# Optimization experiments

Hardware: AMD Instinct MI355X
Metric: run time of the kernel (lower is better)

Reference implementation:

```python
import jax, jax.numpy as jnp
import numpy as np

B, H0, C_IN, C_OUT, K = 8, 32, 512, 512, 3
H1 = 2 * H0  # 64, resolution after bilinear upsample


def _mod_conv(x, conv_w, s):
    """StyleGAN2 modulate+demodulate per-sample conv.
    x: [B,H,W,Cin]; conv_w: [k,k,Cin,Cout]; s: [B,Cout] style scales.
    Implemented as one grouped conv (groups=B) instead of a Python loop.
    """
    wp = conv_w[None] * s[:, None, None, None, :]              # [B,k,k,Cin,Cout]
    d = jax.lax.rsqrt(jnp.sum(wp * wp, axis=(1, 2, 3)) + 1e-8)  # [B,Cout] demod
    wp = wp * d[:, None, None, None, :]
    Bn, H, W, Ci = x.shape
    Co = wp.shape[-1]
    xg = jnp.transpose(x, (1, 2, 0, 3)).reshape(1, H, W, Bn * Ci)
    kg = jnp.transpose(wp, (1, 2, 3, 0, 4)).reshape(wp.shape[1], wp.shape[2], Ci, Bn * Co)
    out = jax.lax.conv_general_dilated(
        xg, kg, (1, 1), 'SAME',
        dimension_numbers=('NHWC', 'HWIO', 'NHWC'),
        feature_group_count=Bn)
    return jnp.transpose(out.reshape(H, W, Bn, Co), (2, 0, 1, 3))


def setup_inputs() -> dict:
    key = jax.random.key(0)
    ks = jax.random.split(key, 13)
    g = 0.02
    return {
        'x': jax.random.uniform(ks[0], (B, H0, H0, C_IN), jnp.float32),
        'w': jax.random.uniform(ks[1], (B, 512), jnp.float32),
        'noise': jax.random.uniform(ks[2], (1, 1, 1, C_OUT), jnp.float32),
        'y0_kernel': jax.random.normal(ks[3], (512, C_OUT), jnp.float32) * g,
        'y0_bias': jnp.zeros((C_OUT,), jnp.float32),
        'y1_kernel': jax.random.normal(ks[4], (512, C_OUT), jnp.float32) * g,
        'y1_bias': jnp.zeros((C_OUT,), jnp.float32),
        'conv0': jax.random.normal(ks[5], (K, K, C_IN, C_OUT), jnp.float32) * g,
        'conv1': jax.random.normal(ks[6], (K, K, C_OUT, C_OUT), jnp.float32) * g,
        'noise_scale0': jax.random.normal(ks[7], (B, H1, H1, C_OUT), jnp.float32) * g,
        'noise_scale1': jax.random.normal(ks[8], (B, H1, H1, C_OUT), jnp.float32) * g,
        'bias0': jax.random.normal(ks[9], (B, H1, H1, C_OUT), jnp.float32) * g,
        'bias1': jax.random.normal(ks[10], (B, H1, H1, C_OUT), jnp.float32) * g,
    }


def reference(x, w, noise, y0_kernel, y0_bias, y1_kernel, y1_bias,
              conv0, conv1, noise_scale0, noise_scale1, bias0, bias1):
    x = jax.image.resize(x, (x.shape[0], 2 * x.shape[1], 2 * x.shape[2], x.shape[3]),
                         method='bilinear')
    s0 = w @ y0_kernel + y0_bias                 # Dense y_0
    x = _mod_conv(x, conv0, s0)
    x = x + noise_scale0 * noise + bias0
    x = jax.nn.leaky_relu(x, 0.2)
    # NOTE: the original TF code computes the second modulated conv but never
    # assigns its result back to x (the tf.concat is missing). We replicate
    # that math faithfully: the conv output is computed and discarded.
    s1 = w @ y1_kernel + y1_bias
    _unused = _mod_conv(x, conv1, s1)
    x = x + noise_scale1 * noise + bias1
    return jax.nn.leaky_relu(x, 0.2)
```

## Files before the change

### kernel.cpp

```cpp
#include <hip/hip_runtime.h>
#include <stdint.h>

typedef __attribute__((ext_vector_type(8))) __bf16 bf16x8;
typedef __attribute__((ext_vector_type(16))) float f32x16;
typedef __attribute__((ext_vector_type(4))) float f32x4;
typedef __attribute__((ext_vector_type(2))) float f32x2;
typedef __attribute__((ext_vector_type(8))) unsigned short us8;

__device__ __forceinline__ unsigned short f2bf(float f) {
  unsigned u = __float_as_uint(f);
  unsigned r = u + 0x7fffu + ((u >> 16) & 1u);
  return (unsigned short)(r >> 16);
}

__device__ __forceinline__ void gload16(const void* gptr, void* lptr) {
  __builtin_amdgcn_global_load_lds(
      (const __attribute__((address_space(1))) void*)gptr,
      (__attribute__((address_space(3))) void*)lptr, 16, 0, 0);
}

__global__ void k_bpack(const float* __restrict__ conv0,
                        unsigned short* __restrict__ bpack,
                        float* __restrict__ wpart) {
  __shared__ float tile[64][65];
  int bx = blockIdx.x;
  int tap = bx >> 6, rem = bx & 63;
  int chunk = rem >> 3, cob = rem & 7;
  int ci0 = chunk << 6, co0 = cob << 6;
  int ty = threadIdx.x >> 6, tx = threadIdx.x & 63;
#pragma unroll
  for (int k = 0; k < 16; ++k) {
    int ci = (k << 2) + ty;
    tile[ci][tx] = conv0[((size_t)(tap * 512 + ci0 + ci)) * 512 + co0 + tx];
  }
  __syncthreads();
  float p = 0.f;
#pragma unroll
  for (int q = 0; q < 16; ++q) {
    float v = tile[(ty << 4) + q][tx];
    p += v * v;
  }
  __shared__ float red[4][64];
  red[ty][tx] = p;
  __syncthreads();
  if (ty == 0)
    wpart[(size_t)(chunk * 9 + tap) * 512 + co0 + tx] =
        red[0][tx] + red[1][tx] + red[2][tx] + red[3][tx];
#pragma unroll
  for (int s2 = 0; s2 < 2; ++s2) {
    int slot = (threadIdx.x << 1) + s2;
    int l = slot & 63;
    int ks = (slot >> 6) & 3;
    int c32l = slot >> 8;
    int col = (c32l << 5) + (l & 31);
    int cil = (ks << 4) + ((l >> 5) << 3);
    us8 o;
#pragma unroll
    for (int e = 0; e < 8; ++e) o[e] = f2bf(tile[cil + e][col]);
    int c32g = (cob << 1) + c32l;
    size_t fi = (((size_t)(chunk * 9 + tap) * 16 + c32g) * 4 + ks);
    *(us8*)(bpack + fi * 512 + (size_t)l * 8) = o;
  }
}

__global__ void k_scale(const float* __restrict__ w, const float* __restrict__ y0k,
                        const float* __restrict__ y0b, const float* __restrict__ wpart,
                        float* __restrict__ scale) {
  int g = blockIdx.x * 256 + threadIdx.x;
  int b = g >> 9, co = g & 511;
  float s = y0b[co];
  const float* wr = w + b * 512;
  for (int ci = 0; ci < 512; ++ci) s += wr[ci] * y0k[ci * 512 + co];
  float ws = 0.f;
  for (int r = 0; r < 72; ++r) ws += wpart[(size_t)r * 512 + co];
  scale[g] = s * rsqrtf(s * s * ws + 1e-8f);
}

__global__ void k_up(const float* __restrict__ x, unsigned short* __restrict__ xpad) {
  int gid = blockIdx.x * 256 + threadIdx.x;
  if (gid >= 8 * 66 * 66 * 64) return;
  int c0 = (gid & 63) << 3;
  int pos = gid >> 6;
  int xx = pos % 66;
  int t = pos / 66;
  int yy = t % 66;
  int b = t / 66;
  unsigned short* dst = xpad + (size_t)pos * 512 + c0;
  us8 o;
  if (yy == 0 || yy == 65 || xx == 0 || xx == 65) {
#pragma unroll
    for (int i = 0; i < 8; ++i) o[i] = 0;
  } else {
    int y = yy - 1, xq = xx - 1;
    int jy = y >> 1, jx = xq >> 1;
    int r0, r1, cx0, cx1;
    float ay0, ay1, ax0, ax1;
    if ((y & 1) == 0) { r0 = jy > 0 ? jy - 1 : 0; r1 = jy;
      ay0 = jy > 0 ? 0.25f : 0.f; ay1 = jy > 0 ? 0.75f : 1.f;
    } else { r0 = jy; r1 = jy < 31 ? jy + 1 : 31;
      ay0 = jy < 31 ? 0.75f : 1.f; ay1 = jy < 31 ? 0.25f : 0.f; }
    if ((xq & 1) == 0) { cx0 = jx > 0 ? jx - 1 : 0; cx1 = jx;
      ax0 = jx > 0 ? 0.25f : 0.f; ax1 = jx > 0 ? 0.75f : 1.f;
    } else { cx0 = jx; cx1 = jx < 31 ? jx + 1 : 31;
      ax0 = jx < 31 ? 0.75f : 1.f; ax1 = jx < 31 ? 0.25f : 0.f; }
    const float* base = x + (size_t)b * 32 * 32 * 512 + c0;
    const f32x4* q00 = (const f32x4*)(base + (size_t)(r0 * 32 + cx0) * 512);
    const f32x4* q01 = (const f32x4*)(base + (size_t)(r0 * 32 + cx1) * 512);
    const f32x4* q10 = (const f32x4*)(base + (size_t)(r1 * 32 + cx0) * 512);
    const f32x4* q11 = (const f32x4*)(base + (size_t)(r1 * 32 + cx1) * 512);
#pragma unroll
    for (int h = 0; h < 2; ++h) {
      f32x4 a = q00[h], bb = q01[h], c = q10[h], d = q11[h];
#pragma unroll
      for (int e = 0; e < 4; ++e) {
        float v = ay0 * (ax0 * a[e] + ax1 * bb[e]) + ay1 * (ax0 * c[e] + ax1 * d[e]);
        o[h * 4 + e] = f2bf(v);
      }
    }
  }
  *(us8*)dst = o;
}

__global__ __launch_bounds__(256) void k_conv(
    const unsigned short* __restrict__ xpad,
    const unsigned short* __restrict__ bpack,
    const float* __restrict__ scale,
    const float* __restrict__ noise,
    const float* __restrict__ ns0, const float* __restrict__ ns1,
    const float* __restrict__ bias0, const float* __restrict__ bias1,
    float* __restrict__ out)
{
  __shared__ __align__(16) unsigned short ldsA[2][16896];

  const int tid = threadIdx.x;
  const int wid = tid >> 6;
  const int lane = tid & 63;
  const int l31 = lane & 31;
  const int lq = (lane >> 5);

  const int bx = blockIdx.x;
  const int nblk = (bx >> 1) & 3;
  const int mblk = ((bx >> 3) << 1) | (bx & 1);
  const int b = mblk >> 5;
  const int y0 = (mblk & 31) << 1;
  const int wr = wid >> 1, wc = wid & 1;
  const int co_base = (nblk << 7) + (wc << 6);

  f32x16 acc[2][2];
#pragma unroll
  for (int i = 0; i < 2; ++i)
#pragma unroll
    for (int n = 0; n < 2; ++n)
#pragma unroll
      for (int e = 0; e < 16; ++e) acc[i][n][e] = 0.f;

  const size_t xb = (size_t)b * (66 * 66 * 512);
  const size_t wboff = (size_t)((nblk << 2) + (wc << 1)) * 2048 + (size_t)lane * 8;
  bf16x8 bq0[8], bq1[8];

  {
#pragma unroll
    for (int i = wid; i < 33; i += 4) {
      int gg = (i << 6) + lane;
      int rx = gg >> 3;
      int r = rx / 66;
      int xx = rx - r * 66;
      int cg = (gg & 7) ^ (xx & 7);
      const unsigned short* src =
          xpad + xb + ((size_t)((y0 + r) * 66 + xx) << 9) + (cg << 3);
      gload16(src, (char*)ldsA[0] + (i << 10));
    }
    const unsigned short* wb = bpack + wboff;
#pragma unroll
    for (int ni = 0; ni < 2; ++ni)
#pragma unroll
      for (int ks = 0; ks < 4; ++ks)
        bq0[ni * 4 + ks] = *(const bf16x8*)(wb + ni * 2048 + ks * 512);
  }
  __syncthreads();

  for (int chunk = 0; chunk < 8; ++chunk) {
    const char* Acur = (const char*)ldsA[chunk & 1];
    const unsigned short* wb = bpack + (size_t)chunk * 294912 + wboff;

#pragma unroll
    for (int tap = 0; tap < 9; ++tap) {
      auto& cur = (tap & 1) ? bq1 : bq0;
      auto& nxt = (tap & 1) ? bq0 : bq1;
      if (tap < 8) {
#pragma unroll
        for (int ni = 0; ni < 2; ++ni)
#pragma unroll
          for (int ks = 0; ks < 4; ++ks)
            nxt[ni * 4 + ks] =
                *(const bf16x8*)(wb + (tap + 1) * 32768 + ni * 2048 + ks * 512);
      } else if (chunk < 7) {
#pragma unroll
        for (int ni = 0; ni < 2; ++ni)
#pragma unroll
          for (int ks = 0; ks < 4; ++ks)
            nxt[ni * 4 + ks] =
                *(const bf16x8*)(wb + 294912 + ni * 2048 + ks * 512);
      }
      if (tap == 0 && chunk < 7) {
        char* Anxt = (char*)ldsA[(chunk + 1) & 1];
        const int kc = (chunk + 1) << 6;
#pragma unroll
        for (int i = wid; i < 33; i += 4) {
          int gg = (i << 6) + lane;
          int rx = gg >> 3;
          int r = rx / 66;
          int xx = rx - r * 66;
          int cg = (gg & 7) ^ (xx & 7);
          const unsigned short* src =
              xpad + xb + ((size_t)((y0 + r) * 66 + xx) << 9) + kc + (cg << 3);
          gload16(src, Anxt + (i << 10));
        }
      }
      const int ky = tap / 3, kx = tap - ky * 3;
      const int r = wr + ky;
      const int axor = ((l31 + kx) & 7) << 4;
#pragma unroll
      for (int ks = 0; ks < 4; ++ks) {
        const int kbyte = (ks << 5) + (lq << 4);
        bf16x8 af[2];
#pragma unroll
        for (int mi = 0; mi < 2; ++mi) {
          int xx = (mi << 5) + l31 + kx;
          int off = ((r * 66 + xx) << 7) + (kbyte ^ axor);
          af[mi] = *(const bf16x8*)(Acur + off);
        }
        __builtin_amdgcn_s_setprio(1);
#pragma unroll
        for (int mi = 0; mi < 2; ++mi)
#pragma unroll
          for (int ni = 0; ni < 2; ++ni)
            acc[mi][ni] = __builtin_amdgcn_mfma_f32_32x32x16_bf16(
                af[mi], cur[ni * 4 + ks], acc[mi][ni], 0, 0, 0);
        __builtin_amdgcn_s_setprio(0);
      }
    }
#pragma unroll
    for (int i = 0; i < 8; ++i) bq0[i] = bq1[i];
    __syncthreads();
  }

  float* ldsE = (float*)ldsA + wid * 4224;
  float sc[2];
#pragma unroll
  for (int ni = 0; ni < 2; ++ni)
    sc[ni] = scale[(b << 9) + co_base + (ni << 5) + l31];
#pragma unroll
  for (int mi = 0; mi < 2; ++mi)
#pragma unroll
    for (int ni = 0; ni < 2; ++ni)
#pragma unroll
      for (int reg = 0; reg < 16; ++reg) {
        int px = (mi << 5) + (reg & 3) + ((reg >> 2) << 3) + (lq << 2);
        ldsE[px * 66 + (ni << 5) + l31] = acc[mi][ni][reg] * sc[ni];
      }
  const int qd = lane & 15;
  const int lhi = lane >> 4;
  const int py = y0 + wr;
  const f32x4 nz4 = *(const f32x4*)(noise + co_base + (qd << 2));
#pragma unroll
  for (int q = 0; q < 16; ++q) {
    int px = (q << 2) + lhi;
    f32x2 v01 = *(const f32x2*)(ldsE + px * 66 + (qd << 2));
    f32x2 v23 = *(const f32x2*)(ldsE + px * 66 + (qd << 2) + 2);
    size_t idx = (((size_t)((b << 6) + py) << 6) + px) * 512 + co_base + (qd << 2);
    f32x4 a0 = *(const f32x4*)(ns0 + idx);
    f32x4 b0 = *(const f32x4*)(bias0 + idx);
    f32x4 a1 = *(const f32x4*)(ns1 + idx);
    f32x4 b1 = *(const f32x4*)(bias1 + idx);
    f32x4 o;
    float vv[4] = {v01[0], v01[1], v23[0], v23[1]};
#pragma unroll
    for (int e = 0; e < 4; ++e) {
      float v0 = vv[e] + a0[e] * nz4[e] + b0[e];
      v0 = fmaxf(v0, 0.2f * v0);
      v0 = v0 + a1[e] * nz4[e] + b1[e];
      o[e] = fmaxf(v0, 0.2f * v0);
    }
    *(f32x4*)(out + idx) = o;
  }
}

extern "C" void kernel_launch(void* const* d_in, const int* in_sizes, int n_in,
                              void* d_out, int out_size, void* d_ws, size_t ws_size,
                              hipStream_t stream) {
  const float* x     = (const float*)d_in[0];
  const float* w     = (const float*)d_in[1];
  const float* noise = (const float*)d_in[2];
  const float* y0k   = (const float*)d_in[3];
  const float* y0b   = (const float*)d_in[4];
  const float* conv0 = (const float*)d_in[7];
  const float* ns0   = (const float*)d_in[9];
  const float* ns1   = (const float*)d_in[10];
  const float* bias0 = (const float*)d_in[11];
  const float* bias1 = (const float*)d_in[12];
  float* out = (float*)d_out;

  char* ws = (char*)d_ws;
  unsigned short* xpad  = (unsigned short*)ws;
  unsigned short* bpack = (unsigned short*)(ws + 35684352);
  float* scale = (float*)(ws + 35684352 + 4718592);
  float* wpart = (float*)(ws + 35684352 + 4718592 + 16384);

  k_bpack<<<576, 256, 0, stream>>>(conv0, bpack, wpart);
  k_scale<<<16, 256, 0, stream>>>(w, y0k, y0b, wpart, scale);
  k_up<<<8712, 256, 0, stream>>>(x, xpad);
  k_conv<<<1024, 256, 0, stream>>>(xpad, bpack, scale, noise, ns0, ns1, bias0, bias1, out);
}
```

Measured before the change: 232.0 us.

## Halve K-chunk to 32 channels to shrink LDS and raise conv occupancy

The conv main loop now walks 16 input-channel chunks of 32 instead of 8 chunks of 64. The A tile in LDS is halved, the swizzle is reworked for 64-byte rows, B fragments per tap drop from 8 to 4 registers, and the weight pack layout is changed to match. The epilogue is split per M-half so it fits the smaller LDS buffer, and launch_bounds(256,4) asks for four blocks per CU. The aim is more resident waves to hide load latency, at the cost of twice as many barriers and LDS staging steps per block.

```diff
diff --git a/kernel.cpp b/kernel.cpp
--- a/kernel.cpp
+++ b/kernel.cpp
@@ -25,8 +25,8 @@
   __shared__ float tile[64][65];
   int bx = blockIdx.x;
   int tap = bx >> 6, rem = bx & 63;
-  int chunk = rem >> 3, cob = rem & 7;
-  int ci0 = chunk << 6, co0 = cob << 6;
+  int chunk64 = rem >> 3, cob = rem & 7;
+  int ci0 = chunk64 << 6, co0 = cob << 6;
   int ty = threadIdx.x >> 6, tx = threadIdx.x & 63;
 #pragma unroll
   for (int k = 0; k < 16; ++k) {
@@ -44,21 +44,22 @@
   red[ty][tx] = p;
   __syncthreads();
   if (ty == 0)
-    wpart[(size_t)(chunk * 9 + tap) * 512 + co0 + tx] =
+    wpart[(size_t)(chunk64 * 9 + tap) * 512 + co0 + tx] =
         red[0][tx] + red[1][tx] + red[2][tx] + red[3][tx];
 #pragma unroll
   for (int s2 = 0; s2 < 2; ++s2) {
     int slot = (threadIdx.x << 1) + s2;
     int l = slot & 63;
-    int ks = (slot >> 6) & 3;
-    int c32l = slot >> 8;
+    int t = slot >> 6;
+    int ks = t & 1, c32l = (t >> 1) & 1, h = t >> 2;
     int col = (c32l << 5) + (l & 31);
-    int cil = (ks << 4) + ((l >> 5) << 3);
+    int cil = (h << 5) + (ks << 4) + ((l >> 5) << 3);
     us8 o;
 #pragma unroll
     for (int e = 0; e < 8; ++e) o[e] = f2bf(tile[cil + e][col]);
+    int chunk16 = (chunk64 << 1) + h;
     int c32g = (cob << 1) + c32l;
-    size_t fi = (((size_t)(chunk * 9 + tap) * 16 + c32g) * 4 + ks);
+    size_t fi = (((size_t)(chunk16 * 9 + tap) * 16 + c32g) << 1) + ks;
     *(us8*)(bpack + fi * 512 + (size_t)l * 8) = o;
   }
 }
@@ -121,7 +122,7 @@
   *(us8*)dst = o;
 }
 
-__global__ __launch_bounds__(256) void k_conv(
+__global__ __launch_bounds__(256, 4) void k_conv(
     const unsigned short* __restrict__ xpad,
     const unsigned short* __restrict__ bpack,
     const float* __restrict__ scale,
@@ -130,13 +131,13 @@
     const float* __restrict__ bias0, const float* __restrict__ bias1,
     float* __restrict__ out)
 {
-  __shared__ __align__(16) unsigned short ldsA[2][16896];
+  __shared__ __align__(16) unsigned short ldsA[2][8448];
 
   const int tid = threadIdx.x;
   const int wid = tid >> 6;
   const int lane = tid & 63;
   const int l31 = lane & 31;
-  const int lq = (lane >> 5);
+  const int lq = lane >> 5;
 
   const int bx = blockIdx.x;
   const int nblk = (bx >> 1) & 3;
@@ -155,33 +156,39 @@
       for (int e = 0; e < 16; ++e) acc[i][n][e] = 0.f;
 
   const size_t xb = (size_t)b * (66 * 66 * 512);
-  const size_t wboff = (size_t)((nblk << 2) + (wc << 1)) * 2048 + (size_t)lane * 8;
-  bf16x8 bq0[8], bq1[8];
-
+  const size_t wboff = ((size_t)((nblk << 2) + (wc << 1)) << 10) + (size_t)lane * 8;
+  bf16x8 bq0[4], bq1[4];
+
+#define STAGE_A(DST, KC)                                                      \
+  {                                                                           \
+    _Pragma("unroll")                                                         \
+    for (int it = 0; it < 5; ++it) {                                          \
+      int g = it * 256 + tid;                                                 \
+      if (it < 4 || tid < 32) {                                               \
+        int rx = g >> 2, c = g & 3;                                           \
+        int r = rx / 66, xx = rx - r * 66;                                    \
+        int cg = c ^ ((xx >> 1) & 3);                                         \
+        const unsigned short* src =                                           \
+            xpad + xb + ((size_t)((y0 + r) * 66 + xx) << 9) + (KC) + (cg << 3);\
+        gload16(src, (char*)(DST) + (g << 4));                                \
+      }                                                                       \
+    }                                                                         \
+  }
+
+  STAGE_A(ldsA[0], 0)
   {
-#pragma unroll
-    for (int i = wid; i < 33; i += 4) {
-      int gg = (i << 6) + lane;
-      int rx = gg >> 3;
-      int r = rx / 66;
-      int xx = rx - r * 66;
-      int cg = (gg & 7) ^ (xx & 7);
-      const unsigned short* src =
-          xpad + xb + ((size_t)((y0 + r) * 66 + xx) << 9) + (cg << 3);
-      gload16(src, (char*)ldsA[0] + (i << 10));
-    }
     const unsigned short* wb = bpack + wboff;
 #pragma unroll
     for (int ni = 0; ni < 2; ++ni)
 #pragma unroll
-      for (int ks = 0; ks < 4; ++ks)
-        bq0[ni * 4 + ks] = *(const bf16x8*)(wb + ni * 2048 + ks * 512);
+      for (int ks = 0; ks < 2; ++ks)
+        bq0[ni * 2 + ks] = *(const bf16x8*)(wb + ni * 1024 + ks * 512);
   }
   __syncthreads();
 
-  for (int chunk = 0; chunk < 8; ++chunk) {
+  for (int chunk = 0; chunk < 16; ++chunk) {
     const char* Acur = (const char*)ldsA[chunk & 1];
-    const unsigned short* wb = bpack + (size_t)chunk * 294912 + wboff;
+    const unsigned short* wb = bpack + (size_t)chunk * 147456 + wboff;
 
 #pragma unroll
     for (int tap = 0; tap < 9; ++tap) {
@@ -191,43 +198,32 @@
 #pragma unroll
         for (int ni = 0; ni < 2; ++ni)
 #pragma unroll
-          for (int ks = 0; ks < 4; ++ks)
-            nxt[ni * 4 + ks] =
-                *(const bf16x8*)(wb + (tap + 1) * 32768 + ni * 2048 + ks * 512);
-      } else if (chunk < 7) {
+          for (int ks = 0; ks < 2; ++ks)
+            nxt[ni * 2 + ks] =
+                *(const bf16x8*)(wb + (tap + 1) * 16384 + ni * 1024 + ks * 512);
+      } else if (chunk < 15) {
 #pragma unroll
         for (int ni = 0; ni < 2; ++ni)
 #pragma unroll
-          for (int ks = 0; ks < 4; ++ks)
-            nxt[ni * 4 + ks] =
-                *(const bf16x8*)(wb + 294912 + ni * 2048 + ks * 512);
-      }
-      if (tap == 0 && chunk < 7) {
+          for (int ks = 0; ks < 2; ++ks)
+            nxt[ni * 2 + ks] =
+                *(const bf16x8*)(wb + 147456 + ni * 1024 + ks * 512);
+      }
+      if (tap == 0 && chunk < 15) {
         char* Anxt = (char*)ldsA[(chunk + 1) & 1];
-        const int kc = (chunk + 1) << 6;
-#pragma unroll
-        for (int i = wid; i < 33; i += 4) {
-          int gg = (i << 6) + lane;
-          int rx = gg >> 3;
-          int r = rx / 66;
-          int xx = rx - r * 66;
-          int cg = (gg & 7) ^ (xx & 7);
-          const unsigned short* src =
-              xpad + xb + ((size_t)((y0 + r) * 66 + xx) << 9) + kc + (cg << 3);
-          gload16(src, Anxt + (i << 10));
-        }
+        const int kc = (chunk + 1) << 5;
+        STAGE_A(Anxt, kc)
       }
       const int ky = tap / 3, kx = tap - ky * 3;
       const int r = wr + ky;
-      const int axor = ((l31 + kx) & 7) << 4;
-#pragma unroll
-      for (int ks = 0; ks < 4; ++ks) {
-        const int kbyte = (ks << 5) + (lq << 4);
+#pragma unroll
+      for (int ks = 0; ks < 2; ++ks) {
         bf16x8 af[2];
 #pragma unroll
         for (int mi = 0; mi < 2; ++mi) {
           int xx = (mi << 5) + l31 + kx;
-          int off = ((r * 66 + xx) << 7) + (kbyte ^ axor);
+          int slot = ((ks << 1) | lq) ^ ((xx >> 1) & 3);
+          int off = ((r * 66 + xx) << 6) + (slot << 4);
           af[mi] = *(const bf16x8*)(Acur + off);
         }
         __builtin_amdgcn_s_setprio(1);
@@ -236,54 +232,57 @@
 #pragma unroll
           for (int ni = 0; ni < 2; ++ni)
             acc[mi][ni] = __builtin_amdgcn_mfma_f32_32x32x16_bf16(
-                af[mi], cur[ni * 4 + ks], acc[mi][ni], 0, 0, 0);
+                af[mi], cur[ni * 2 + ks], acc[mi][ni], 0, 0, 0);
         __builtin_amdgcn_s_setprio(0);
       }
     }
 #pragma unroll
-    for (int i = 0; i < 8; ++i) bq0[i] = bq1[i];
+    for (int i = 0; i < 4; ++i) bq0[i] = bq1[i];
     __syncthreads();
   }
 
-  float* ldsE = (float*)ldsA + wid * 4224;
+  float* ldsE = (float*)ldsA + wid * 2112;
   float sc[2];
 #pragma unroll
   for (int ni = 0; ni < 2; ++ni)
     sc[ni] = scale[(b << 9) + co_base + (ni << 5) + l31];
-#pragma unroll
-  for (int mi = 0; mi < 2; ++mi)
-#pragma unroll
-    for (int ni = 0; ni < 2; ++ni)
-#pragma unroll
-      for (int reg = 0; reg < 16; ++reg) {
-        int px = (mi << 5) + (reg & 3) + ((reg >> 2) << 3) + (lq << 2);
-        ldsE[px * 66 + (ni << 5) + l31] = acc[mi][ni][reg] * sc[ni];
-      }
   const int qd = lane & 15;
   const int lhi = lane >> 4;
   const int py = y0 + wr;
   const f32x4 nz4 = *(const f32x4*)(noise + co_base + (qd << 2));
 #pragma unroll
-  for (int q = 0; q < 16; ++q) {
-    int px = (q << 2) + lhi;
-    f32x2 v01 = *(const f32x2*)(ldsE + px * 66 + (qd << 2));
-    f32x2 v23 = *(const f32x2*)(ldsE + px * 66 + (qd << 2) + 2);
-    size_t idx = (((size_t)((b << 6) + py) << 6) + px) * 512 + co_base + (qd << 2);
-    f32x4 a0 = *(const f32x4*)(ns0 + idx);
-    f32x4 b0 = *(const f32x4*)(bias0 + idx);
-    f32x4 a1 = *(const f32x4*)(ns1 + idx);
-    f32x4 b1 = *(const f32x4*)(bias1 + idx);
-    f32x4 o;
-    float vv[4] = {v01[0], v01[1], v23[0], v23[1]};
-#pragma unroll
-    for (int e = 0; e < 4; ++e) {
-      float v0 = vv[e] + a0[e] * nz4[e] + b0[e];
-      v0 = fmaxf(v0, 0.2f * v0);
-      v0 = v0 + a1[e] * nz4[e] + b1[e];
-      o[e] = fmaxf(v0, 0.2f * v0);
+  for (int mi = 0; mi < 2; ++mi) {
+#pragma unroll
+    for (int ni = 0; ni < 2; ++ni)
+#pragma unroll
+      for (int reg = 0; reg < 16; ++reg) {
+        int row = (reg & 3) + ((reg >> 2) << 3) + (lq << 2);
+        ldsE[row * 66 + (ni << 5) + l31] = acc[mi][ni][reg] * sc[ni];
+      }
+#pragma unroll
+    for (int q = 0; q < 8; ++q) {
+      int pxl = (q << 2) + lhi;
+      int xcol = (mi << 5) + pxl;
+      f32x2 v01 = *(const f32x2*)(ldsE + pxl * 66 + (qd << 2));
+      f32x2 v23 = *(const f32x2*)(ldsE + pxl * 66 + (qd << 2) + 2);
+      size_t idx = (((size_t)((b << 6) + py) << 6) + xcol) * 512 + co_base + (qd << 2);
+      f32x4 a0 = *(const f32x4*)(ns0 + idx);
+      f32x4 b0 = *(const f32x4*)(bias0 + idx);
+      f32x4 a1 = *(const f32x4*)(ns1 + idx);
+      f32x4 b1 = *(const f32x4*)(bias1 + idx);
+      f32x4 o;
+      float vv[4] = {v01[0], v01[1], v23[0], v23[1]};
+#pragma unroll
+      for (int e = 0; e < 4; ++e) {
+        float v0 = vv[e] + a0[e] * nz4[e] + b0[e];
+        v0 = fmaxf(v0, 0.2f * v0);
+        v0 = v0 + a1[e] * nz4[e] + b1[e];
+        o[e] = fmaxf(v0, 0.2f * v0);
+      }
+      *(f32x4*)(out + idx) = o;
     }
-    *(f32x4*)(out + idx) = o;
-  }
+  }
+#undef STAGE_A
 }
 
 extern "C" void kernel_launch(void* const* d_in, const int* in_sizes, int n_in,
```

Result: slower. 294.5 us (+26.9%).

## Widen conv block tile to 256 channels with 8 waves and finer B prefetch

Applied to the files above, without the earlier changes.

Restructures the implicit-GEMM conv kernel so each 512-thread block covers 2 rows by 256 output channels, with 8 waves each owning 32 pixels by 128 channels. The same staged input tile in LDS is now reused across twice as many output channels, and the A-staging load is spread over all threads. B-fragment prefetch moves from per-tap to per-k-step double buffering, which shrinks the register footprint so that four blocks per SM can be requested. The block-to-tile mapping is remapped for L2 locality. The epilogue is split into two passes to fit the smaller per-wave LDS scratch area. Risks include halving the grid to 512 blocks, which may reduce occupancy balance across CUs, and more frequent, smaller global B loads per MFMA.

```diff
diff --git a/kernel.cpp b/kernel.cpp
--- a/kernel.cpp
+++ b/kernel.cpp
@@ -121,7 +121,7 @@
   *(us8*)dst = o;
 }
 
-__global__ __launch_bounds__(256) void k_conv(
+__global__ __launch_bounds__(512, 4) void k_conv(
     const unsigned short* __restrict__ xpad,
     const unsigned short* __restrict__ bpack,
     const float* __restrict__ scale,
@@ -136,46 +136,52 @@
   const int wid = tid >> 6;
   const int lane = tid & 63;
   const int l31 = lane & 31;
-  const int lq = (lane >> 5);
+  const int lq = lane >> 5;
 
   const int bx = blockIdx.x;
-  const int nblk = (bx >> 1) & 3;
-  const int mblk = ((bx >> 3) << 1) | (bx & 1);
+  const int g8 = bx & 7, j = bx >> 3;
+  const int nblk = g8 & 1;
+  const int mblk = ((g8 >> 1) << 6) + j;
   const int b = mblk >> 5;
   const int y0 = (mblk & 31) << 1;
-  const int wr = wid >> 1, wc = wid & 1;
-  const int co_base = (nblk << 7) + (wc << 6);
-
-  f32x16 acc[2][2];
-#pragma unroll
-  for (int i = 0; i < 2; ++i)
-#pragma unroll
-    for (int n = 0; n < 2; ++n)
-#pragma unroll
-      for (int e = 0; e < 16; ++e) acc[i][n][e] = 0.f;
+
+  const int wc = wid & 1;
+  const int xh32 = ((wid >> 1) & 1) << 5;
+  const int rb = wid >> 2;
+  const int co_base = (nblk << 8) + (wc << 7);
+
+  f32x16 acc[4];
+#pragma unroll
+  for (int n = 0; n < 4; ++n)
+#pragma unroll
+    for (int e = 0; e < 16; ++e) acc[n][e] = 0.f;
 
   const size_t xb = (size_t)b * (66 * 66 * 512);
-  const size_t wboff = (size_t)((nblk << 2) + (wc << 1)) * 2048 + (size_t)lane * 8;
-  bf16x8 bq0[8], bq1[8];
-
+  const size_t wboff = ((size_t)((nblk << 3) + (wc << 2)) << 11) + (size_t)lane * 8;
+  bf16x8 bqA[4], bqB[4];
+
+#define STAGE_A(DST, KC)                                                       \
+  {                                                                            \
+    _Pragma("unroll")                                                          \
+    for (int it = 0; it < 5; ++it) {                                           \
+      int g = it * 512 + tid;                                                  \
+      if (it < 4 || tid < 64) {                                                \
+        int rpx = g >> 3, sl = g & 7;                                          \
+        int r = rpx / 66, px = rpx - r * 66;                                   \
+        int ci = ((sl ^ (px & 7)) << 3) + (KC);                                \
+        const unsigned short* src =                                            \
+            xpad + xb + ((size_t)((y0 + r) * 66 + px) << 9) + ci;              \
+        gload16(src, (char*)(DST) + (g << 4));                                 \
+      }                                                                        \
+    }                                                                          \
+  }
+
+  STAGE_A(ldsA[0], 0)
   {
-#pragma unroll
-    for (int i = wid; i < 33; i += 4) {
-      int gg = (i << 6) + lane;
-      int rx = gg >> 3;
-      int r = rx / 66;
-      int xx = rx - r * 66;
-      int cg = (gg & 7) ^ (xx & 7);
-      const unsigned short* src =
-          xpad + xb + ((size_t)((y0 + r) * 66 + xx) << 9) + (cg << 3);
-      gload16(src, (char*)ldsA[0] + (i << 10));
-    }
     const unsigned short* wb = bpack + wboff;
 #pragma unroll
-    for (int ni = 0; ni < 2; ++ni)
-#pragma unroll
-      for (int ks = 0; ks < 4; ++ks)
-        bq0[ni * 4 + ks] = *(const bf16x8*)(wb + ni * 2048 + ks * 512);
+    for (int ni = 0; ni < 4; ++ni)
+      bqA[ni] = *(const bf16x8*)(wb + ni * 2048);
   }
   __syncthreads();
 
@@ -185,105 +191,94 @@
 
 #pragma unroll
     for (int tap = 0; tap < 9; ++tap) {
-      auto& cur = (tap & 1) ? bq1 : bq0;
-      auto& nxt = (tap & 1) ? bq0 : bq1;
-      if (tap < 8) {
-#pragma unroll
-        for (int ni = 0; ni < 2; ++ni)
-#pragma unroll
-          for (int ks = 0; ks < 4; ++ks)
-            nxt[ni * 4 + ks] =
-                *(const bf16x8*)(wb + (tap + 1) * 32768 + ni * 2048 + ks * 512);
-      } else if (chunk < 7) {
-#pragma unroll
-        for (int ni = 0; ni < 2; ++ni)
-#pragma unroll
-          for (int ks = 0; ks < 4; ++ks)
-            nxt[ni * 4 + ks] =
-                *(const bf16x8*)(wb + 294912 + ni * 2048 + ks * 512);
-      }
+      const int ky = tap / 3, kx = tap - ky * 3;
+      const int r = rb + ky;
+      const int px = xh32 + l31 + kx;
+      const int rowoff = (r * 66 + px) << 7;
+      const int psl = px & 7;
+      bf16x8 af[4];
+#pragma unroll
+      for (int ks = 0; ks < 4; ++ks)
+        af[ks] = *(const bf16x8*)(Acur + rowoff + ((((ks << 1) | lq) ^ psl) << 4));
       if (tap == 0 && chunk < 7) {
         char* Anxt = (char*)ldsA[(chunk + 1) & 1];
         const int kc = (chunk + 1) << 6;
-#pragma unroll
-        for (int i = wid; i < 33; i += 4) {
-          int gg = (i << 6) + lane;
-          int rx = gg >> 3;
-          int r = rx / 66;
-          int xx = rx - r * 66;
-          int cg = (gg & 7) ^ (xx & 7);
-          const unsigned short* src =
-              xpad + xb + ((size_t)((y0 + r) * 66 + xx) << 9) + kc + (cg << 3);
-          gload16(src, Anxt + (i << 10));
-        }
-      }
-      const int ky = tap / 3, kx = tap - ky * 3;
-      const int r = wr + ky;
-      const int axor = ((l31 + kx) & 7) << 4;
+        STAGE_A(Anxt, kc)
+      }
 #pragma unroll
       for (int ks = 0; ks < 4; ++ks) {
-        const int kbyte = (ks << 5) + (lq << 4);
-        bf16x8 af[2];
-#pragma unroll
-        for (int mi = 0; mi < 2; ++mi) {
-          int xx = (mi << 5) + l31 + kx;
-          int off = ((r * 66 + xx) << 7) + (kbyte ^ axor);
-          af[mi] = *(const bf16x8*)(Acur + off);
+        bf16x8* cur = (ks & 1) ? bqB : bqA;
+        bf16x8* nxt = (ks & 1) ? bqA : bqB;
+        if (ks < 3) {
+#pragma unroll
+          for (int ni = 0; ni < 4; ++ni)
+            nxt[ni] = *(const bf16x8*)(wb + tap * 32768 + ni * 2048 + (ks + 1) * 512);
+        } else if (tap < 8) {
+#pragma unroll
+          for (int ni = 0; ni < 4; ++ni)
+            nxt[ni] = *(const bf16x8*)(wb + (tap + 1) * 32768 + ni * 2048);
+        } else if (chunk < 7) {
+#pragma unroll
+          for (int ni = 0; ni < 4; ++ni)
+            nxt[ni] = *(const bf16x8*)(wb + 294912 + ni * 2048);
         }
         __builtin_amdgcn_s_setprio(1);
 #pragma unroll
-        for (int mi = 0; mi < 2; ++mi)
-#pragma unroll
-          for (int ni = 0; ni < 2; ++ni)
-            acc[mi][ni] = __builtin_amdgcn_mfma_f32_32x32x16_bf16(
-                af[mi], cur[ni * 4 + ks], acc[mi][ni], 0, 0, 0);
+        for (int ni = 0; ni < 4; ++ni)
+          acc[ni] = __builtin_amdgcn_mfma_f32_32x32x16_bf16(
+              af[ks], cur[ni], acc[ni], 0, 0, 0);
         __builtin_amdgcn_s_setprio(0);
       }
     }
-#pragma unroll
-    for (int i = 0; i < 8; ++i) bq0[i] = bq1[i];
     __syncthreads();
   }
 
-  float* ldsE = (float*)ldsA + wid * 4224;
-  float sc[2];
-#pragma unroll
-  for (int ni = 0; ni < 2; ++ni)
+  __syncthreads();
+  float* ldsE = (float*)ldsA + wid * 2112;
+  float sc[4];
+#pragma unroll
+  for (int ni = 0; ni < 4; ++ni)
     sc[ni] = scale[(b << 9) + co_base + (ni << 5) + l31];
-#pragma unroll
-  for (int mi = 0; mi < 2; ++mi)
-#pragma unroll
-    for (int ni = 0; ni < 2; ++ni)
-#pragma unroll
-      for (int reg = 0; reg < 16; ++reg) {
-        int px = (mi << 5) + (reg & 3) + ((reg >> 2) << 3) + (lq << 2);
-        ldsE[px * 66 + (ni << 5) + l31] = acc[mi][ni][reg] * sc[ni];
-      }
   const int qd = lane & 15;
   const int lhi = lane >> 4;
-  const int py = y0 + wr;
-  const f32x4 nz4 = *(const f32x4*)(noise + co_base + (qd << 2));
-#pragma unroll
-  for (int q = 0; q < 16; ++q) {
-    int px = (q << 2) + lhi;
-    f32x2 v01 = *(const f32x2*)(ldsE + px * 66 + (qd << 2));
-    f32x2 v23 = *(const f32x2*)(ldsE + px * 66 + (qd << 2) + 2);
-    size_t idx = (((size_t)((b << 6) + py) << 6) + px) * 512 + co_base + (qd << 2);
-    f32x4 a0 = *(const f32x4*)(ns0 + idx);
-    f32x4 b0 = *(const f32x4*)(bias0 + idx);
-    f32x4 a1 = *(const f32x4*)(ns1 + idx);
-    f32x4 b1 = *(const f32x4*)(bias1 + idx);
-    f32x4 o;
-    float vv[4] = {v01[0], v01[1], v23[0], v23[1]};
-#pragma unroll
-    for (int e = 0; e < 4; ++e) {
-      float v0 = vv[e] + a0[e] * nz4[e] + b0[e];
-      v0 = fmaxf(v0, 0.2f * v0);
-      v0 = v0 + a1[e] * nz4[e] + b1[e];
-      o[e] = fmaxf(v0, 0.2f * v0);
+  const int row = y0 + rb;
+#pragma unroll
+  for (int p = 0; p < 2; ++p) {
+#pragma unroll
+    for (int n2 = 0; n2 < 2; ++n2) {
+      int ni = (p << 1) + n2;
+#pragma unroll
+      for (int reg = 0; reg < 16; ++reg) {
+        int pxrow = (reg & 3) + ((reg >> 2) << 3) + (lq << 2);
+        ldsE[pxrow * 66 + (n2 << 5) + l31] = acc[ni][reg] * sc[ni];
+      }
     }
-    *(f32x4*)(out + idx) = o;
-  }
+    const int cpass = co_base + (p << 6);
+    const f32x4 nz4 = *(const f32x4*)(noise + cpass + (qd << 2));
+#pragma unroll
+    for (int q = 0; q < 8; ++q) {
+      int pxl = (q << 2) + lhi;
+      int xcol = xh32 + pxl;
+      f32x2 v01 = *(const f32x2*)(ldsE + pxl * 66 + (qd << 2));
+      f32x2 v23 = *(const f32x2*)(ldsE + pxl * 66 + (qd << 2) + 2);
+      size_t idx = (((size_t)((b << 6) + row) << 6) + xcol) * 512 + cpass + (qd << 2);
+      f32x4 a0 = *(const f32x4*)(ns0 + idx);
+      f32x4 b0 = *(const f32x4*)(bias0 + idx);
+      f32x4 a1 = *(const f32x4*)(ns1 + idx);
+      f32x4 b1 = *(const f32x4*)(bias1 + idx);
+      f32x4 o;
+      float vv[4] = {v01[0], v01[1], v23[0], v23[1]};
+#pragma unroll
+      for (int e = 0; e < 4; ++e) {
+        float v0 = vv[e] + a0[e] * nz4[e] + b0[e];
+        v0 = fmaxf(v0, 0.2f * v0);
+        v0 = v0 + a1[e] * nz4[e] + b1[e];
+        o[e] = fmaxf(v0, 0.2f * v0);
+      }
+      *(f32x4*)(out + idx) = o;
+    }
+  }
+#undef STAGE_A
 }
 
 extern "C" void kernel_launch(void* const* d_in, const int* in_sizes, int n_in,
@@ -310,5 +305,5 @@
   k_bpack<<<576, 256, 0, stream>>>(conv0, bpack, wpart);
   k_scale<<<16, 256, 0, stream>>>(w, y0k, y0b, wpart, scale);
   k_up<<<8712, 256, 0, stream>>>(x, xpad);
-  k_conv<<<1024, 256, 0, stream>>>(xpad, bpack, scale, noise, ns0, ns1, bias0, bias1, out);
-}
+  k_conv<<<512, 512, 0, stream>>>(xpad, bpack, scale, noise, ns0, ns1, bias0, bias1, out);
+}
```

Result: slower. 339.1 us (+46.2%).
